# Kernel tuning notes

Measured on AMD Instinct MI355X. Metric: run time of the kernel, lower is better.

Reference implementation:

```python
import jax, jax.numpy as jnp
import numpy as np

B, S, DIM = 8, 1024, 192
D2 = 2 * DIM            # inner width 384
CH = 4                  # cell heads (= qk_size)
HD = D2 // CH           # 96 head dim
NB = D2 // 4            # 96 block-diagonal blocks
BLK = D2 // NB          # block size 4
TAU = float(HD) ** 0.5


def setup_inputs() -> dict:
    key = jax.random.key(0)
    ks = jax.random.split(key, 16)
    r = lambda i, shp, s=0.02: jax.random.normal(ks[i], shp, jnp.float32) * s
    return {
        "x": jax.random.normal(ks[0], (B, S, DIM), jnp.float32),
        "ln_g": jnp.ones((DIM,), jnp.float32), "ln_b": jnp.zeros((DIM,), jnp.float32),
        "w1": r(1, (D2, DIM)), "b1": jnp.zeros((D2,), jnp.float32),
        "w2": r(2, (D2, DIM)), "b2": jnp.zeros((D2,), jnp.float32),
        "conv_w": r(3, (D2, 1, 3), 0.1), "conv_b": jnp.zeros((D2,), jnp.float32),
        "qw": r(4, (NB, BLK, BLK), 0.1), "qb": jnp.zeros((D2,), jnp.float32),
        "kw": r(5, (NB, BLK, BLK), 0.1), "kb": jnp.zeros((D2,), jnp.float32),
        "vw": r(6, (NB, BLK, BLK), 0.1), "vb": jnp.zeros((D2,), jnp.float32),
        "wi": r(7, (CH, 3 * D2)), "bi": jax.random.normal(ks[8], (CH,), jnp.float32) * 0.1,
        "wf": r(9, (CH, 3 * D2)), "bf": jnp.linspace(3.0, 6.0, CH).astype(jnp.float32),
        "gn_g": jnp.ones((D2,), jnp.float32), "gn_b": jnp.zeros((D2,), jnp.float32),
        "wo": r(10, (DIM, D2)), "bo": jnp.zeros((DIM,), jnp.float32),
        "skip": jnp.ones((D2,), jnp.float32),
    }


def _layernorm(x, g, b):
    m = x.mean(-1, keepdims=True)
    v = ((x - m) ** 2).mean(-1, keepdims=True)
    return (x - m) / jnp.sqrt(v + 1e-5) * g + b


def _blockdiag(x, w, b):
    # x: [B,S,D2] -> blocks [B,S,NB,BLK]; w: [NB, out_blk, in_blk]
    bs, sq, _ = x.shape
    y = jnp.einsum('bsni,noi->bsno', x.reshape(bs, sq, NB, BLK), w)
    return y.reshape(bs, sq, D2) + b


def _dwconv(x, w, b):
    # depthwise conv over sequence: x [B,S,C] -> [B,C,S] conv -> [B,S,C]
    y = jax.lax.conv_general_dilated(
        x.transpose(0, 2, 1), w, window_strides=(1,), padding=[(1, 1)],
        dimension_numbers=('NCH', 'OIH', 'NCH'), feature_group_count=D2)
    return y.transpose(0, 2, 1) + b


def _cell(q, k, v, wi, bi, wf, bf, gn_g, gn_b):
    bs, sq, _ = q.shape
    gi = jnp.concatenate([q, k, v], axis=-1)                      # [B,S,3*D2]
    it = jnp.einsum('bsc,hc->bhs', gi, wi) + bi[None, :, None]    # [B,H,S]
    ft = jnp.einsum('bsc,hc->bhs', gi, wf) + bf[None, :, None]
    c = jnp.cumsum(jax.nn.log_sigmoid(ft), axis=-1)               # [B,H,S]
    logm = c[..., :, None] - c[..., None, :]                      # cum[i]-cum[j]
    mask = jnp.tril(jnp.ones((sq, sq), dtype=bool))
    f_act = jnp.where(mask, logm, -jnp.inf)
    dt = f_act + it[:, :, None, :]                                # add itilde over cols
    max_d = jnp.max(dt, axis=-1, keepdims=True)
    dmat = jnp.exp(dt - max_d)                                    # [B,H,S,S]
    qh = q.reshape(bs, sq, CH, HD).transpose(0, 2, 1, 3)
    kh = k.reshape(bs, sq, CH, HD).transpose(0, 2, 1, 3)
    vh = v.reshape(bs, sq, CH, HD).transpose(0, 2, 1, 3)
    ct = jnp.einsum('bhid,bhjd->bhij', qh, kh) * dmat / TAU
    maxit = jnp.maximum(jnp.abs(ct.sum(-1, keepdims=True)), jnp.exp(-max_d))
    h = jnp.einsum('bhij,bhjd->bhid', ct, vh) / (maxit + 1e-6)
    h = h.transpose(0, 2, 1, 3).reshape(bs, sq, CH, HD)           # per-token GroupNorm
    mu = h.mean(-1, keepdims=True)
    var = ((h - mu) ** 2).mean(-1, keepdims=True)
    h = (h - mu) / jnp.sqrt(var + 1e-5)
    h = h * gn_g.reshape(CH, HD) + gn_b.reshape(CH, HD)
    return h.reshape(bs, sq, D2)


def reference(x, ln_g, ln_b, w1, b1, w2, b2, conv_w, conv_b, qw, qb, kw, kb,
              vw, vb, wi, bi, wf, bf, gn_g, gn_b, wo, bo, skip):
    inputs = _layernorm(x, ln_g, ln_b)
    a = inputs @ w1.T + b1                   # [B,S,D2]
    bgate = jax.nn.silu(inputs @ w2.T + b2)  # [B,S,D2]
    qk = jax.nn.silu(_dwconv(a, conv_w, conv_b))
    q = _blockdiag(qk, qw, qb)
    k = _blockdiag(qk, kw, kb)
    v = _blockdiag(a, vw, vb)
    out1 = _cell(q, k, v, wi, bi, wf, bf, gn_g, gn_b)
    out1 = (out1 + skip * qk) * bgate
    out = out1 @ wo.T + bo
    return out + x
```

## Files before the change

### kernel.cpp

```cpp
#include <hip/hip_runtime.h>
#include <cstdint>

#define TAU_ 9.797958971132712f

typedef __attribute__((ext_vector_type(4))) float f32x4;
typedef __attribute__((ext_vector_type(8))) short short8;

#define DEV static __device__ __forceinline__

DEV unsigned short f2bf(float f){
  union { float f; unsigned u; } v; v.f = f;
  unsigned r = v.u + 0x7FFFu + ((v.u >> 16) & 1u);
  return (unsigned short)(r >> 16);
}
DEV float bf2f(unsigned short u){
  union { unsigned u; float f; } v; v.u = ((unsigned)u) << 16; return v.f;
}
DEV unsigned pack2bf(float a, float b){
  unsigned r;
  asm("v_cvt_pk_bf16_f32 %0, %1, %2" : "=v"(r) : "v"(a), "v"(b));
  return r;
}
DEV f32x4 ld_bf4(const unsigned short* p){
  uint2 r = *(const uint2*)p;
  f32x4 o;
  o[0] = bf2f((unsigned short)(r.x & 0xffff));
  o[1] = bf2f((unsigned short)(r.x >> 16));
  o[2] = bf2f((unsigned short)(r.y & 0xffff));
  o[3] = bf2f((unsigned short)(r.y >> 16));
  return o;
}
DEV float siluf_(float x){ return x / (1.f + __expf(-x)); }
DEV float logsigf_(float x){ return fminf(x, 0.f) - log1pf(__expf(-fabsf(x))); }

__global__ __launch_bounds__(256) void k1a_ln(
    const float* __restrict__ x, const float* __restrict__ ln_g, const float* __restrict__ ln_b,
    short* __restrict__ xnbf)
{
  const int tid = threadIdx.x;
  const int t = blockIdx.x * 16 + (tid >> 4);
  const int g = tid & 15;
  const float* xr = x + (long)t * 192 + g * 12;
  f32x4 v0 = *(const f32x4*)(xr);
  f32x4 v1 = *(const f32x4*)(xr + 4);
  f32x4 v2 = *(const f32x4*)(xr + 8);
  float s  = v0[0]+v0[1]+v0[2]+v0[3] + v1[0]+v1[1]+v1[2]+v1[3] + v2[0]+v2[1]+v2[2]+v2[3];
  float sq = v0[0]*v0[0]+v0[1]*v0[1]+v0[2]*v0[2]+v0[3]*v0[3]
           + v1[0]*v1[0]+v1[1]*v1[1]+v1[2]*v1[2]+v1[3]*v1[3]
           + v2[0]*v2[0]+v2[1]*v2[1]+v2[2]*v2[2]+v2[3]*v2[3];
  s  += __shfl_xor(s, 1);  s  += __shfl_xor(s, 2);  s  += __shfl_xor(s, 4);  s  += __shfl_xor(s, 8);
  sq += __shfl_xor(sq, 1); sq += __shfl_xor(sq, 2); sq += __shfl_xor(sq, 4); sq += __shfl_xor(sq, 8);
  const float mean = s * (1.f/192.f);
  const float rstd = rsqrtf(sq * (1.f/192.f) - mean * mean + 1e-5f);
  const int c0 = g * 12;
  f32x4 g0 = *(const f32x4*)(ln_g + c0),     b0 = *(const f32x4*)(ln_b + c0);
  f32x4 g1 = *(const f32x4*)(ln_g + c0 + 4), b1 = *(const f32x4*)(ln_b + c0 + 4);
  f32x4 g2 = *(const f32x4*)(ln_g + c0 + 8), b2 = *(const f32x4*)(ln_b + c0 + 8);
  unsigned pk[6];
  pk[0] = pack2bf((v0[0]-mean)*rstd*g0[0]+b0[0], (v0[1]-mean)*rstd*g0[1]+b0[1]);
  pk[1] = pack2bf((v0[2]-mean)*rstd*g0[2]+b0[2], (v0[3]-mean)*rstd*g0[3]+b0[3]);
  pk[2] = pack2bf((v1[0]-mean)*rstd*g1[0]+b1[0], (v1[1]-mean)*rstd*g1[1]+b1[1]);
  pk[3] = pack2bf((v1[2]-mean)*rstd*g1[2]+b1[2], (v1[3]-mean)*rstd*g1[3]+b1[3]);
  pk[4] = pack2bf((v2[0]-mean)*rstd*g2[0]+b2[0], (v2[1]-mean)*rstd*g2[1]+b2[1]);
  pk[5] = pack2bf((v2[2]-mean)*rstd*g2[2]+b2[2], (v2[3]-mean)*rstd*g2[3]+b2[3]);
  uint2* xo = (uint2*)(xnbf + (long)t * 192 + g * 12);
  xo[0] = make_uint2(pk[0], pk[1]);
  xo[1] = make_uint2(pk[2], pk[3]);
  xo[2] = make_uint2(pk[4], pk[5]);
}

__global__ __launch_bounds__(256) void k1b_gemm(
    const short* __restrict__ xnbf,
    const float* __restrict__ w1, const float* __restrict__ w2,
    const float* __restrict__ b1, const float* __restrict__ b2,
    unsigned short* __restrict__ abf, unsigned short* __restrict__ bgate)
{
  __shared__ short wt[18432];
  const int tid = threadIdx.x;
  const int ntg = blockIdx.x & 7;
  const int t0 = (blockIdx.x >> 3) * 64;
  {
    const float* src = (ntg < 4 ? w1 : w2) + (long)(ntg & 3) * 96 * 192;
    #pragma unroll
    for(int i = 0; i < 9; i++){
      const int u = i * 256 + tid;
      const int row = u / 24;
      const int dst = (u * 16) ^ ((row & 7) << 4);
      f32x4 f0 = *(const f32x4*)(src + u * 8);
      f32x4 f1 = *(const f32x4*)(src + u * 8 + 4);
      uint4 pk;
      pk.x = pack2bf(f0[0], f0[1]); pk.y = pack2bf(f0[2], f0[3]);
      pk.z = pack2bf(f1[0], f1[1]); pk.w = pack2bf(f1[2], f1[3]);
      *(uint4*)((char*)wt + dst) = pk;
    }
  }
  __syncthreads();
  const int widx = tid >> 6, lane = tid & 63, qg = lane >> 4, l16 = lane & 15;
  const int mrow = widx * 16 + l16;
  f32x4 acc[6];
  #pragma unroll
  for(int nt = 0; nt < 6; nt++) acc[nt] = (f32x4){0.f,0.f,0.f,0.f};
  const short* xrow = xnbf + (long)(t0 + mrow) * 192;
  #pragma unroll
  for(int kc = 0; kc < 6; kc++){
    short8 af = *(const short8*)(xrow + kc * 32 + 8 * qg);
    #pragma unroll
    for(int nt = 0; nt < 6; nt++){
      const int row = nt * 16 + l16;
      int byte = row * 384 + (kc * 32 + 8 * qg) * 2;
      byte ^= (row & 7) << 4;
      short8 bfr = *(const short8*)((const char*)wt + byte);
      acc[nt] = __builtin_amdgcn_mfma_f32_16x16x32_bf16(af, bfr, acc[nt], 0, 0, 0);
    }
  }
  const int half = ntg >> 2;
  const float* bias = half ? b2 : b1;
  const int ncol = (ntg & 3) * 96;
  #pragma unroll
  for(int nt = 0; nt < 6; nt++){
    const int n = ncol + nt * 16 + l16;
    const float bs = bias[n];
    #pragma unroll
    for(int r = 0; r < 4; r++){
      const int trow = t0 + widx * 16 + 4 * qg + r;
      float v = acc[nt][r] + bs;
      if(half) bgate[(long)trow * 384 + n] = f2bf(siluf_(v));
      else     abf[(long)trow * 384 + n] = f2bf(v);
    }
  }
}

__global__ __launch_bounds__(256) void k2bv(
    const unsigned short* __restrict__ abf,
    const float* __restrict__ cw, const float* __restrict__ cb,
    const float* __restrict__ qw, const float* __restrict__ qb,
    const float* __restrict__ kw, const float* __restrict__ kb,
    const float* __restrict__ vw, const float* __restrict__ vb,
    unsigned short* __restrict__ qkbf, short* __restrict__ qbf, short* __restrict__ kbf,
    short* __restrict__ vtbf)
{
  __shared__ float vt[64][97];
  const int tid = threadIdx.x;
  const int bh = blockIdx.x >> 4;
  const int b = bh >> 2, h = bh & 3;
  const int s0 = (blockIdx.x & 15) << 6;
  #pragma unroll
  for(int it = 0; it < 6; it++){
    const int f = it * 256 + tid;
    const int sl = f / 24, c4l = f % 24;
    const int c4 = h * 24 + c4l;
    const int s = s0 + sl;
    const long t = (long)b * 1024 + s;
    const long abase = t * 384 + c4 * 4;
    f32x4 am = ld_bf4(abf + abase);
    f32x4 al = (s > 0)    ? ld_bf4(abf + abase - 384) : (f32x4){0.f,0.f,0.f,0.f};
    f32x4 ar = (s < 1023) ? ld_bf4(abf + abase + 384) : (f32x4){0.f,0.f,0.f,0.f};
    f32x4 cw0 = *(const f32x4*)(cw + c4 * 12);
    f32x4 cw1 = *(const f32x4*)(cw + c4 * 12 + 4);
    f32x4 cw2 = *(const f32x4*)(cw + c4 * 12 + 8);
    f32x4 cb4 = *(const f32x4*)(cb + c4 * 4);
    f32x4 in;
    in[0] = siluf_(cb4[0] + al[0]*cw0[0] + am[0]*cw0[1] + ar[0]*cw0[2]);
    in[1] = siluf_(cb4[1] + al[1]*cw0[3] + am[1]*cw1[0] + ar[1]*cw1[1]);
    in[2] = siluf_(cb4[2] + al[2]*cw1[2] + am[2]*cw1[3] + ar[2]*cw2[0]);
    in[3] = siluf_(cb4[3] + al[3]*cw2[1] + am[3]*cw2[2] + ar[3]*cw2[3]);
    {
      uint2 pk; pk.x = pack2bf(in[0], in[1]); pk.y = pack2bf(in[2], in[3]);
      *(uint2*)(qkbf + abase) = pk;
    }
    const long base = ((long)(b * 4 + h) * 1024 + s) * 96 + c4l * 4;
    {
      const float* w = qw + c4 * 16;
      float v0 = qb[c4*4+0] + w[0]*in[0]  + w[1]*in[1]  + w[2]*in[2]  + w[3]*in[3];
      float v1 = qb[c4*4+1] + w[4]*in[0]  + w[5]*in[1]  + w[6]*in[2]  + w[7]*in[3];
      float v2 = qb[c4*4+2] + w[8]*in[0]  + w[9]*in[1]  + w[10]*in[2] + w[11]*in[3];
      float v3 = qb[c4*4+3] + w[12]*in[0] + w[13]*in[1] + w[14]*in[2] + w[15]*in[3];
      uint2 pk; pk.x = pack2bf(v0, v1); pk.y = pack2bf(v2, v3);
      *(uint2*)(qbf + base) = pk;
    }
    {
      const float* w = kw + c4 * 16;
      float v0 = kb[c4*4+0] + w[0]*in[0]  + w[1]*in[1]  + w[2]*in[2]  + w[3]*in[3];
      float v1 = kb[c4*4+1] + w[4]*in[0]  + w[5]*in[1]  + w[6]*in[2]  + w[7]*in[3];
      float v2 = kb[c4*4+2] + w[8]*in[0]  + w[9]*in[1]  + w[10]*in[2] + w[11]*in[3];
      float v3 = kb[c4*4+3] + w[12]*in[0] + w[13]*in[1] + w[14]*in[2] + w[15]*in[3];
      uint2 pk; pk.x = pack2bf(v0, v1); pk.y = pack2bf(v2, v3);
      *(uint2*)(kbf + base) = pk;
    }
    {
      const float* w = vw + c4 * 16;
      #pragma unroll
      for(int o = 0; o < 4; o++){
        float v = vb[c4*4+o] + w[o*4]*am[0] + w[o*4+1]*am[1] + w[o*4+2]*am[2] + w[o*4+3]*am[3];
        vt[sl][c4l * 4 + o] = v;
      }
    }
  }
  __syncthreads();
  #pragma unroll
  for(int it = 0; it < 24; it++){
    const int f = it * 256 + tid;
    const int d = f >> 6, sl = f & 63;
    vtbf[((long)bh * 96 + d) * 1024 + s0 + sl] = (short)f2bf(vt[sl][d]);
  }
}

__global__ __launch_bounds__(256) void k2c_gates(
    const short* __restrict__ qbf, const short* __restrict__ kbf,
    const unsigned short* __restrict__ abf,
    const float* __restrict__ vw, const float* __restrict__ vb,
    const float* __restrict__ wi, const float* __restrict__ bi,
    const float* __restrict__ wf, const float* __restrict__ bff,
    float* __restrict__ itv, float* __restrict__ ftv)
{
  const int tid = threadIdx.x;
  const int lane = tid & 63, widx = tid >> 6;
  const int t = blockIdx.x * 4 + widx;
  const int b = t >> 10, s = t & 1023;
  float pit[4] = {0,0,0,0}, pft[4] = {0,0,0,0};
  for(int j = 0; j < 18; j++){
    const int e = lane + 64 * j;
    float val;
    if(e < 768){
      const int c = (e >= 384) ? e - 384 : e;
      const short* src = (e >= 384) ? kbf : qbf;
      const int h = c / 96, d = c - h * 96;
      val = bf2f((unsigned short)src[((long)(b * 4 + h) * 1024 + s) * 96 + d]);
    } else {
      const int c = e - 768;
      const int c4 = c >> 2, o = c & 3;
      f32x4 in = ld_bf4(abf + (long)t * 384 + c4 * 4);
      const float* w = vw + c4 * 16 + o * 4;
      val = vb[c] + w[0]*in[0] + w[1]*in[1] + w[2]*in[2] + w[3]*in[3];
    }
    #pragma unroll
    for(int h = 0; h < 4; h++){
      pit[h] += val * wi[h * 1152 + e];
      pft[h] += val * wf[h * 1152 + e];
    }
  }
  #pragma unroll
  for(int h = 0; h < 4; h++){
    float vi = pit[h], vf = pft[h];
    #pragma unroll
    for(int m = 1; m < 64; m <<= 1){ vi += __shfl_xor(vi, m); vf += __shfl_xor(vf, m); }
    if(lane == 0){
      itv[((long)(b * 4 + h)) * 1024 + s] = vi + bi[h];
      ftv[((long)(b * 4 + h)) * 1024 + s] = vf + bff[h];
    }
  }
}

__global__ __launch_bounds__(256) void k3_scan(
    const float* __restrict__ itv, const float* __restrict__ ftv,
    float* __restrict__ Ev, float* __restrict__ Rpv, float* __restrict__ dsv)
{
  __shared__ float sb[256];
  const int bh = blockIdx.x, tid = threadIdx.x;
  const long base = (long)bh * 1024 + tid * 4;
  f32x4 f4 = *(const f32x4*)(ftv + base);
  const float l0 = logsigf_(f4[0]);
  const float l1 = logsigf_(f4[1]);
  const float l2 = logsigf_(f4[2]);
  const float l3 = logsigf_(f4[3]);
  float c0 = l0, c1 = l0 + l1, c2 = c1 + l2, c3 = c2 + l3;
  sb[tid] = c3;
  __syncthreads();
  for(int off = 1; off < 256; off <<= 1){
    float mine = sb[tid];
    float oth = (tid >= off) ? sb[tid - off] : 0.f;
    __syncthreads();
    sb[tid] = mine + oth;
    __syncthreads();
  }
  const float excl = (tid > 0) ? sb[tid - 1] : 0.f;
  c0 += excl; c1 += excl; c2 += excl; c3 += excl;
  f32x4 i4 = *(const f32x4*)(itv + base);
  const float m0 = i4[0] - c0, m1 = i4[1] - c1, m2 = i4[2] - c2, m3 = i4[3] - c3;
  const float x1 = fmaxf(m0, m1), x2 = fmaxf(x1, m2), x3 = fmaxf(x2, m3);
  __syncthreads();
  sb[tid] = x3;
  __syncthreads();
  for(int off = 1; off < 256; off <<= 1){
    float mine = sb[tid];
    float oth = (tid >= off) ? sb[tid - off] : -3.4e38f;
    __syncthreads();
    sb[tid] = fmaxf(mine, oth);
    __syncthreads();
  }
  const float exm = (tid > 0) ? sb[tid - 1] : -3.4e38f;
  const float M0 = fmaxf(m0, exm);
  const float M1 = fmaxf(x1, exm);
  const float M2 = fmaxf(x2, exm);
  const float M3 = fmaxf(x3, exm);
  f32x4 e, rp, ds;
  e[0] = __expf(m0); e[1] = __expf(m1); e[2] = __expf(m2); e[3] = __expf(m3);
  rp[0] = __expf(-M0) * (1.f/TAU_); rp[1] = __expf(-M1) * (1.f/TAU_);
  rp[2] = __expf(-M2) * (1.f/TAU_); rp[3] = __expf(-M3) * (1.f/TAU_);
  ds[0] = __expf(-(c0 + M0)); ds[1] = __expf(-(c1 + M1));
  ds[2] = __expf(-(c2 + M2)); ds[3] = __expf(-(c3 + M3));
  *(f32x4*)(Ev  + base) = e;
  *(f32x4*)(Rpv + base) = rp;
  *(f32x4*)(dsv + base) = ds;
}

__global__ __launch_bounds__(256, 2) void k4_attn(
    const short* __restrict__ qbf, const short* __restrict__ kbf, const short* __restrict__ vtbf,
    const float* __restrict__ Ev, const float* __restrict__ Rpv, const float* __restrict__ dsv,
    const float* __restrict__ gn_g, const float* __restrict__ gn_b,
    const unsigned short* __restrict__ qkbf, const unsigned short* __restrict__ bgate,
    const float* __restrict__ skip, short* __restrict__ o1bf)
{
  __shared__ short kbuf[2][64 * 104];
  __shared__ short vbuf[2][96 * 72];
  __shared__ float ebuf[2][64];
  __shared__ short P[4][16][72];
  const int tid = threadIdx.x;
  const int w = tid >> 6, lane = tid & 63, qg = lane >> 4, l16 = lane & 15;
  const int xcd = blockIdx.x & 7, q = blockIdx.x >> 3;
  const int bh = ((q & 3) << 3) | xcd;
  const int qh = q >> 2;
  const int ib = (q < 32) ? (15 - qh) : (qh - 8);
  const int i0w = ib * 64 + w * 16;
  const long qkbase = (long)bh * 1024;
  const int nj = ib + 1;

  short8 qf[3];
  #pragma unroll
  for(int kc = 0; kc < 3; kc++)
    qf[kc] = *(const short8*)(qbf + (qkbase + i0w + l16) * 96 + kc * 32 + 8 * qg);
  const float rp = Rpv[qkbase + i0w + l16];
  const float ds = dsv[qkbase + i0w + l16];

  f32x4 acc[6];
  #pragma unroll
  for(int dt = 0; dt < 6; dt++) acc[dt] = (f32x4){0.f,0.f,0.f,0.f};
  float bp = 0.f;

  const int rK0 = tid / 12,        cK0 = tid % 12;
  const int rK1 = (tid+256) / 12,  cK1 = (tid+256) % 12;
  const int rK2 = (tid+512) / 12,  cK2 = (tid+512) % 12;
  const int dV0 = tid >> 3,        cV0 = tid & 7;
  const int dV1 = (tid+256) >> 3,  cV1 = (tid+256) & 7;
  const int dV2 = (tid+512) >> 3,  cV2 = (tid+512) & 7;
  const bool he = (tid < 16);
  short8 sk0, sk1, sk2, sv0, sv1, sv2; f32x4 se;
  const short* kgb = kbf + qkbase * 96;
  const short* vgb = vtbf + (long)bh * 96 * 1024;

#define STAGE_LOAD(J0)                                              \
  {                                                                 \
    const int j0_ = (J0);                                           \
    sk0 = *(const short8*)(kgb + (j0_ + rK0) * 96 + cK0 * 8);       \
    sk1 = *(const short8*)(kgb + (j0_ + rK1) * 96 + cK1 * 8);       \
    sk2 = *(const short8*)(kgb + (j0_ + rK2) * 96 + cK2 * 8);       \
    sv0 = *(const short8*)(vgb + (long)dV0 * 1024 + j0_ + cV0 * 8); \
    sv1 = *(const short8*)(vgb + (long)dV1 * 1024 + j0_ + cV1 * 8); \
    sv2 = *(const short8*)(vgb + (long)dV2 * 1024 + j0_ + cV2 * 8); \
    if(he) se = *(const f32x4*)(Ev + qkbase + j0_ + tid * 4);       \
  }

#define STAGE_WRITE(B)                                   \
  {                                                      \
    *(short8*)(&kbuf[B][rK0 * 104 + cK0 * 8]) = sk0;     \
    *(short8*)(&kbuf[B][rK1 * 104 + cK1 * 8]) = sk1;     \
    *(short8*)(&kbuf[B][rK2 * 104 + cK2 * 8]) = sk2;     \
    *(short8*)(&vbuf[B][dV0 * 72 + cV0 * 8]) = sv0;      \
    *(short8*)(&vbuf[B][dV1 * 72 + cV1 * 8]) = sv1;      \
    *(short8*)(&vbuf[B][dV2 * 72 + cV2 * 8]) = sv2;      \
    if(he) *(f32x4*)(&ebuf[B][tid * 4]) = se;            \
  }

  STAGE_LOAD(0);
  int cur = 0;
  for(int jt = 0; jt < nj; jt++){
    STAGE_WRITE(cur);
    __syncthreads();
    if(jt + 1 < nj) STAGE_LOAD((jt + 1) * 64);

    const int j0 = jt * 64;
    const bool diag = (jt == nj - 1);
    const int i = i0w + l16;
    __builtin_amdgcn_s_setprio(1);
    #pragma unroll
    for(int jsub = 0; jsub < 4; jsub++){
      f32x4 C = (f32x4){0.f,0.f,0.f,0.f};
      #pragma unroll
      for(int kc = 0; kc < 3; kc++){
        short8 kf = *(const short8*)(&kbuf[cur][(jsub*16 + l16) * 104 + kc * 32 + 8 * qg]);
        C = __builtin_amdgcn_mfma_f32_16x16x32_bf16(kf, qf[kc], C, 0, 0, 0);
      }
      f32x4 e4 = *(const f32x4*)(&ebuf[cur][jsub * 16 + 4 * qg]);
      float v0 = C[0] * e4[0];
      float v1 = C[1] * e4[1];
      float v2 = C[2] * e4[2];
      float v3 = C[3] * e4[3];
      if(diag){
        const int jb = j0 + jsub * 16 + 4 * qg;
        if(jb + 0 > i) v0 = 0.f;
        if(jb + 1 > i) v1 = 0.f;
        if(jb + 2 > i) v2 = 0.f;
        if(jb + 3 > i) v3 = 0.f;
      }
      bp += v0 + v1 + v2 + v3;
      uint2 pw; pw.x = pack2bf(v0, v1); pw.y = pack2bf(v2, v3);
      *(uint2*)(&P[w][l16][jsub * 16 + 4 * qg]) = pw;
    }
    asm volatile("s_waitcnt lgkmcnt(0)" ::: "memory");
    #pragma unroll
    for(int ksub = 0; ksub < 2; ksub++){
      short8 pa = *(const short8*)(&P[w][l16][ksub * 32 + 8 * qg]);
      #pragma unroll
      for(int dt = 0; dt < 6; dt++){
        short8 vf = *(const short8*)(&vbuf[cur][(dt * 16 + l16) * 72 + ksub * 32 + 8 * qg]);
        acc[dt] = __builtin_amdgcn_mfma_f32_16x16x32_bf16(pa, vf, acc[dt], 0, 0, 0);
      }
    }
    __builtin_amdgcn_s_setprio(0);
    cur ^= 1;
  }
#undef STAGE_LOAD
#undef STAGE_WRITE

  const int head = bh & 3, bb = bh >> 2;
  float bsum = bp;
  bsum += __shfl_xor(bsum, 16);
  bsum += __shfl_xor(bsum, 32);
  const float bfull = bsum * rp;
  const float den = fmaxf(fabsf(bfull), ds) + 1e-6f;
  const float sc = rp / den;
  float srow[4];
  #pragma unroll
  for(int r = 0; r < 4; r++) srow[r] = __shfl(sc, 4 * qg + r);
  float hv[6][4], mu[4], rs[4];
  #pragma unroll
  for(int r = 0; r < 4; r++){
    float sm = 0.f, sq = 0.f;
    #pragma unroll
    for(int dt = 0; dt < 6; dt++){
      const float h = acc[dt][r] * srow[r];
      hv[dt][r] = h; sm += h; sq += h * h;
    }
    sm += __shfl_xor(sm, 1); sm += __shfl_xor(sm, 2); sm += __shfl_xor(sm, 4); sm += __shfl_xor(sm, 8);
    sq += __shfl_xor(sq, 1); sq += __shfl_xor(sq, 2); sq += __shfl_xor(sq, 4); sq += __shfl_xor(sq, 8);
    const float m_ = sm * (1.f/96.f);
    mu[r] = m_;
    rs[r] = rsqrtf(sq * (1.f/96.f) - m_ * m_ + 1e-5f);
  }
  __syncthreads();
  short* hstage = &kbuf[0][0];
  #pragma unroll
  for(int dt = 0; dt < 6; dt++){
    const int col = head * 96 + dt * 16 + l16;
    const float g  = gn_g[col];
    const float be = gn_b[col];
    #pragma unroll
    for(int r = 0; r < 4; r++){
      const float hn = (hv[dt][r] - mu[r]) * rs[r] * g + be;
      hstage[(w * 16 + 4 * qg + r) * 104 + dt * 16 + l16] = (short)f2bf(hn);
    }
  }
  __syncthreads();
  #pragma unroll
  for(int u2 = 0; u2 < 3; u2++){
    const int f = u2 * 256 + tid;
    const int row = f / 12, c8 = f % 12;
    const long off = ((long)(bb * 1024 + ib * 64 + row)) * 384 + head * 96 + c8 * 8;
    short8 h8 = *(const short8*)(hstage + row * 104 + c8 * 8);
    short8 q8 = *(const short8*)((const short*)qkbf + off);
    short8 g8 = *(const short8*)((const short*)bgate + off);
    f32x4 s0 = *(const f32x4*)(skip + head * 96 + c8 * 8);
    f32x4 s1 = *(const f32x4*)(skip + head * 96 + c8 * 8 + 4);
    float o[8];
    #pragma unroll
    for(int i = 0; i < 8; i++){
      const float sk = (i < 4) ? s0[i] : s1[i - 4];
      o[i] = (bf2f((unsigned short)h8[i]) + sk * bf2f((unsigned short)q8[i]))
             * bf2f((unsigned short)g8[i]);
    }
    union { short8 s; unsigned u4[4]; } ov;
    ov.u4[0] = pack2bf(o[0], o[1]); ov.u4[1] = pack2bf(o[2], o[3]);
    ov.u4[2] = pack2bf(o[4], o[5]); ov.u4[3] = pack2bf(o[6], o[7]);
    *(short8*)(o1bf + off) = ov.s;
  }
}

__global__ __launch_bounds__(256) void k5_gemm(
    const short* __restrict__ o1bf, const float* __restrict__ wo,
    const float* __restrict__ bo, const float* __restrict__ x, float* __restrict__ out)
{
  __shared__ short wt[18432];
  const int tid = threadIdx.x;
  const int ng = blockIdx.x & 3;
  const int t0 = (blockIdx.x >> 2) * 64;
  {
    const float* src = wo + (long)ng * 48 * 384;
    #pragma unroll
    for(int i = 0; i < 9; i++){
      const int u = i * 256 + tid;
      const int row = u / 48;
      const int dst = (u * 16) ^ ((row & 7) << 4);
      f32x4 f0 = *(const f32x4*)(src + u * 8);
      f32x4 f1 = *(const f32x4*)(src + u * 8 + 4);
      uint4 pk;
      pk.x = pack2bf(f0[0], f0[1]); pk.y = pack2bf(f0[2], f0[3]);
      pk.z = pack2bf(f1[0], f1[1]); pk.w = pack2bf(f1[2], f1[3]);
      *(uint4*)((char*)wt + dst) = pk;
    }
  }
  __syncthreads();
  const int widx = tid >> 6, lane = tid & 63, qg = lane >> 4, l16 = lane & 15;
  f32x4 acc[3];
  #pragma unroll
  for(int nt = 0; nt < 3; nt++) acc[nt] = (f32x4){0.f,0.f,0.f,0.f};
  const short* arow = o1bf + (long)(t0 + widx * 16 + l16) * 384;
  #pragma unroll
  for(int kc = 0; kc < 12; kc++){
    short8 af = *(const short8*)(arow + kc * 32 + 8 * qg);
    #pragma unroll
    for(int nt = 0; nt < 3; nt++){
      const int row = nt * 16 + l16;
      int byte = row * 768 + kc * 64 + qg * 16;
      byte ^= (row & 7) << 4;
      short8 bfr = *(const short8*)((const char*)wt + byte);
      acc[nt] = __builtin_amdgcn_mfma_f32_16x16x32_bf16(af, bfr, acc[nt], 0, 0, 0);
    }
  }
  #pragma unroll
  for(int nt = 0; nt < 3; nt++){
    const int n = ng * 48 + nt * 16 + l16;
    const float b_ = bo[n];
    #pragma unroll
    for(int r = 0; r < 4; r++){
      const int trow = t0 + widx * 16 + 4 * qg + r;
      out[(long)trow * 192 + n] = acc[nt][r] + b_ + x[(long)trow * 192 + n];
    }
  }
}

extern "C" void kernel_launch(void* const* d_in, const int* in_sizes, int n_in,
                              void* d_out, int out_size, void* d_ws, size_t ws_size,
                              hipStream_t stream)
{
  (void)in_sizes; (void)n_in; (void)out_size; (void)ws_size;
  const float* x    = (const float*)d_in[0];
  const float* ln_g = (const float*)d_in[1];
  const float* ln_b = (const float*)d_in[2];
  const float* w1   = (const float*)d_in[3];
  const float* b1   = (const float*)d_in[4];
  const float* w2   = (const float*)d_in[5];
  const float* b2   = (const float*)d_in[6];
  const float* cw   = (const float*)d_in[7];
  const float* cb   = (const float*)d_in[8];
  const float* qw   = (const float*)d_in[9];
  const float* qb   = (const float*)d_in[10];
  const float* kw   = (const float*)d_in[11];
  const float* kb   = (const float*)d_in[12];
  const float* vw   = (const float*)d_in[13];
  const float* vb   = (const float*)d_in[14];
  const float* wi   = (const float*)d_in[15];
  const float* bi   = (const float*)d_in[16];
  const float* wf   = (const float*)d_in[17];
  const float* bff  = (const float*)d_in[18];
  const float* gn_g = (const float*)d_in[19];
  const float* gn_b = (const float*)d_in[20];
  const float* wo   = (const float*)d_in[21];
  const float* bo   = (const float*)d_in[22];
  const float* skip = (const float*)d_in[23];
  float* out = (float*)d_out;

  char* ws = (char*)d_ws;
  unsigned short* abf   = (unsigned short*)(ws + 0);
  unsigned short* bgate = (unsigned short*)(ws + 12582912);
  unsigned short* qkbf  = (unsigned short*)(ws + 25165824);
  short* xnbf  = (short*)(ws + 37748736);
  short* o1bf  = (short*)(ws + 41943040);
  short* qbf   = (short*)(ws + 50331648);
  short* kbf   = (short*)(ws + 56623104);
  short* vtbf  = (short*)(ws + 62914560);
  float* itv   = (float*)(ws + 69648384);
  float* ftv   = (float*)(ws + 69779456);
  float* Ev    = (float*)(ws + 69910528);
  float* Rpv   = (float*)(ws + 70041600);
  float* dsv   = (float*)(ws + 70172672);

  k1a_ln<<<512, 256, 0, stream>>>(x, ln_g, ln_b, xnbf);
  k1b_gemm<<<1024, 256, 0, stream>>>(xnbf, w1, w2, b1, b2, abf, bgate);
  k2bv<<<512, 256, 0, stream>>>(abf, cw, cb, qw, qb, kw, kb, vw, vb, qkbf, qbf, kbf, vtbf);
  k2c_gates<<<2048, 256, 0, stream>>>(qbf, kbf, abf, vw, vb, wi, bi, wf, bff, itv, ftv);
  k3_scan<<<32, 256, 0, stream>>>(itv, ftv, Ev, Rpv, dsv);
  k4_attn<<<512, 256, 0, stream>>>(qbf, kbf, vtbf, Ev, Rpv, dsv, gn_g, gn_b,
                                   qkbf, bgate, skip, o1bf);
  k5_gemm<<<512, 256, 0, stream>>>(o1bf, wo, bo, x, out);
}
```

Measured before the change: 89.10 us.

## Single-buffer K/V LDS tiles in attention kernel and raise occupancy to four blocks

Drops the double-buffered K, V and E shared-memory tiles in the attention kernel in favour of a single buffer. A second barrier at the end of each tile iteration keeps the next write from overwriting data still being read. This roughly halves the LDS footprint, and launch bounds are raised to four blocks per CU so more waves can hide latency. The cost is an extra __syncthreads per tile and a tighter register budget, which may cause spills. Global prefetch into registers still overlaps with compute.

```diff
diff --git a/kernel.cpp b/kernel.cpp
--- a/kernel.cpp
+++ b/kernel.cpp
@@ -304,16 +304,16 @@
   *(f32x4*)(dsv + base) = ds;
 }
 
-__global__ __launch_bounds__(256, 2) void k4_attn(
+__global__ __launch_bounds__(256, 4) void k4_attn(
     const short* __restrict__ qbf, const short* __restrict__ kbf, const short* __restrict__ vtbf,
     const float* __restrict__ Ev, const float* __restrict__ Rpv, const float* __restrict__ dsv,
     const float* __restrict__ gn_g, const float* __restrict__ gn_b,
     const unsigned short* __restrict__ qkbf, const unsigned short* __restrict__ bgate,
     const float* __restrict__ skip, short* __restrict__ o1bf)
 {
-  __shared__ short kbuf[2][64 * 104];
-  __shared__ short vbuf[2][96 * 72];
-  __shared__ float ebuf[2][64];
+  __shared__ short kbuf[64 * 104];
+  __shared__ short vbuf[96 * 72];
+  __shared__ float ebuf[64];
   __shared__ short P[4][16][72];
   const int tid = threadIdx.x;
   const int w = tid >> 6, lane = tid & 63, qg = lane >> 4, l16 = lane & 15;
@@ -360,21 +360,20 @@
     if(he) se = *(const f32x4*)(Ev + qkbase + j0_ + tid * 4);       \
   }
 
-#define STAGE_WRITE(B)                                   \
+#define STAGE_WRITE()                                    \
   {                                                      \
-    *(short8*)(&kbuf[B][rK0 * 104 + cK0 * 8]) = sk0;     \
-    *(short8*)(&kbuf[B][rK1 * 104 + cK1 * 8]) = sk1;     \
-    *(short8*)(&kbuf[B][rK2 * 104 + cK2 * 8]) = sk2;     \
-    *(short8*)(&vbuf[B][dV0 * 72 + cV0 * 8]) = sv0;      \
-    *(short8*)(&vbuf[B][dV1 * 72 + cV1 * 8]) = sv1;      \
-    *(short8*)(&vbuf[B][dV2 * 72 + cV2 * 8]) = sv2;      \
-    if(he) *(f32x4*)(&ebuf[B][tid * 4]) = se;            \
+    *(short8*)(&kbuf[rK0 * 104 + cK0 * 8]) = sk0;        \
+    *(short8*)(&kbuf[rK1 * 104 + cK1 * 8]) = sk1;        \
+    *(short8*)(&kbuf[rK2 * 104 + cK2 * 8]) = sk2;        \
+    *(short8*)(&vbuf[dV0 * 72 + cV0 * 8]) = sv0;         \
+    *(short8*)(&vbuf[dV1 * 72 + cV1 * 8]) = sv1;         \
+    *(short8*)(&vbuf[dV2 * 72 + cV2 * 8]) = sv2;         \
+    if(he) *(f32x4*)(&ebuf[tid * 4]) = se;               \
   }
 
   STAGE_LOAD(0);
-  int cur = 0;
   for(int jt = 0; jt < nj; jt++){
-    STAGE_WRITE(cur);
+    STAGE_WRITE();
     __syncthreads();
     if(jt + 1 < nj) STAGE_LOAD((jt + 1) * 64);
 
@@ -387,10 +386,10 @@
       f32x4 C = (f32x4){0.f,0.f,0.f,0.f};
       #pragma unroll
       for(int kc = 0; kc < 3; kc++){
-        short8 kf = *(const short8*)(&kbuf[cur][(jsub*16 + l16) * 104 + kc * 32 + 8 * qg]);
+        short8 kf = *(const short8*)(&kbuf[(jsub*16 + l16) * 104 + kc * 32 + 8 * qg]);
         C = __builtin_amdgcn_mfma_f32_16x16x32_bf16(kf, qf[kc], C, 0, 0, 0);
       }
-      f32x4 e4 = *(const f32x4*)(&ebuf[cur][jsub * 16 + 4 * qg]);
+      f32x4 e4 = *(const f32x4*)(&ebuf[jsub * 16 + 4 * qg]);
       float v0 = C[0] * e4[0];
       float v1 = C[1] * e4[1];
       float v2 = C[2] * e4[2];
@@ -412,12 +411,12 @@
       short8 pa = *(const short8*)(&P[w][l16][ksub * 32 + 8 * qg]);
       #pragma unroll
       for(int dt = 0; dt < 6; dt++){
-        short8 vf = *(const short8*)(&vbuf[cur][(dt * 16 + l16) * 72 + ksub * 32 + 8 * qg]);
+        short8 vf = *(const short8*)(&vbuf[(dt * 16 + l16) * 72 + ksub * 32 + 8 * qg]);
         acc[dt] = __builtin_amdgcn_mfma_f32_16x16x32_bf16(pa, vf, acc[dt], 0, 0, 0);
       }
     }
     __builtin_amdgcn_s_setprio(0);
-    cur ^= 1;
+    __syncthreads();
   }
 #undef STAGE_LOAD
 #undef STAGE_WRITE
@@ -447,8 +446,7 @@
     mu[r] = m_;
     rs[r] = rsqrtf(sq * (1.f/96.f) - m_ * m_ + 1e-5f);
   }
-  __syncthreads();
-  short* hstage = &kbuf[0][0];
+  short* hstage = &kbuf[0];
   #pragma unroll
   for(int dt = 0; dt < 6; dt++){
     const int col = head * 96 + dt * 16 + l16;
```

After: 93.51 us. +5.0%, slower.

## Compute gate projections with bf16 MFMA and a materialized V buffer

Applied to the files above, without the earlier changes.

The gate kernel, which had one wave per token doing scalar dot products and shuffle reductions, is rewritten to use 16x16x32 bf16 MFMA. Each block loads the wi/wf gate weights into LDS as bf16 and covers 64 tokens. To feed it, k2bv now also writes the block-diagonal V projection to a token-major bf16 buffer, so the gate kernel no longer recomputes V from `a`. In exchange, k2bv writes one extra buffer, the grid shrinks to 128 blocks, and the V values and gate weights are rounded to bf16 inside the gate computation.

```diff
diff --git a/kernel.cpp b/kernel.cpp
--- a/kernel.cpp
+++ b/kernel.cpp
@@ -137,7 +137,7 @@
     const float* __restrict__ kw, const float* __restrict__ kb,
     const float* __restrict__ vw, const float* __restrict__ vb,
     unsigned short* __restrict__ qkbf, short* __restrict__ qbf, short* __restrict__ kbf,
-    short* __restrict__ vtbf)
+    short* __restrict__ vbf, short* __restrict__ vtbf)
 {
   __shared__ float vt[64][97];
   const int tid = threadIdx.x;
@@ -189,11 +189,15 @@
     }
     {
       const float* w = vw + c4 * 16;
+      float vv[4];
       #pragma unroll
       for(int o = 0; o < 4; o++){
         float v = vb[c4*4+o] + w[o*4]*am[0] + w[o*4+1]*am[1] + w[o*4+2]*am[2] + w[o*4+3]*am[3];
+        vv[o] = v;
         vt[sl][c4l * 4 + o] = v;
       }
+      uint2 pk; pk.x = pack2bf(vv[0], vv[1]); pk.y = pack2bf(vv[2], vv[3]);
+      *(uint2*)(vbf + abase) = pk;
     }
   }
   __syncthreads();
@@ -206,47 +210,48 @@
 }
 
 __global__ __launch_bounds__(256) void k2c_gates(
-    const short* __restrict__ qbf, const short* __restrict__ kbf,
-    const unsigned short* __restrict__ abf,
-    const float* __restrict__ vw, const float* __restrict__ vb,
+    const short* __restrict__ qbf, const short* __restrict__ kbf, const short* __restrict__ vbf,
     const float* __restrict__ wi, const float* __restrict__ bi,
     const float* __restrict__ wf, const float* __restrict__ bff,
     float* __restrict__ itv, float* __restrict__ ftv)
 {
+  __shared__ short wg[8 * 1160];
   const int tid = threadIdx.x;
-  const int lane = tid & 63, widx = tid >> 6;
-  const int t = blockIdx.x * 4 + widx;
-  const int b = t >> 10, s = t & 1023;
-  float pit[4] = {0,0,0,0}, pft[4] = {0,0,0,0};
-  for(int j = 0; j < 18; j++){
-    const int e = lane + 64 * j;
-    float val;
-    if(e < 768){
-      const int c = (e >= 384) ? e - 384 : e;
-      const short* src = (e >= 384) ? kbf : qbf;
-      const int h = c / 96, d = c - h * 96;
-      val = bf2f((unsigned short)src[((long)(b * 4 + h) * 1024 + s) * 96 + d]);
-    } else {
-      const int c = e - 768;
-      const int c4 = c >> 2, o = c & 3;
-      f32x4 in = ld_bf4(abf + (long)t * 384 + c4 * 4);
-      const float* w = vw + c4 * 16 + o * 4;
-      val = vb[c] + w[0]*in[0] + w[1]*in[1] + w[2]*in[2] + w[3]*in[3];
-    }
-    #pragma unroll
-    for(int h = 0; h < 4; h++){
-      pit[h] += val * wi[h * 1152 + e];
-      pft[h] += val * wf[h * 1152 + e];
-    }
-  }
-  #pragma unroll
-  for(int h = 0; h < 4; h++){
-    float vi = pit[h], vf = pft[h];
-    #pragma unroll
-    for(int m = 1; m < 64; m <<= 1){ vi += __shfl_xor(vi, m); vf += __shfl_xor(vf, m); }
-    if(lane == 0){
-      itv[((long)(b * 4 + h)) * 1024 + s] = vi + bi[h];
-      ftv[((long)(b * 4 + h)) * 1024 + s] = vf + bff[h];
+  const int t0 = blockIdx.x * 64;
+  #pragma unroll
+  for(int i = 0; i < 9; i++){
+    const int u = i * 256 + tid;
+    const int row = u / 288, col4 = u % 288;
+    const float* src = ((row < 4) ? wi + row * 1152 : wf + (row - 4) * 1152) + col4 * 4;
+    f32x4 v = *(const f32x4*)src;
+    uint2 pk; pk.x = pack2bf(v[0], v[1]); pk.y = pack2bf(v[2], v[3]);
+    *(uint2*)(&wg[row * 1160 + col4 * 4]) = pk;
+  }
+  __syncthreads();
+  const int w = tid >> 6, lane = tid & 63, qg = lane >> 4, l16 = lane & 15;
+  const int tw = t0 + w * 16;
+  const int tA = tw + l16;
+  const int b = tA >> 10, s = tA & 1023;
+  f32x4 acc = (f32x4){0.f,0.f,0.f,0.f};
+  #pragma unroll
+  for(int kc = 0; kc < 36; kc++){
+    const int blk = kc / 3;
+    const int off = (kc % 3) * 32 + qg * 8;
+    short8 af;
+    if(blk < 4)      af = *(const short8*)(qbf + ((long)(b*4+blk)*1024 + s)*96 + off);
+    else if(blk < 8) af = *(const short8*)(kbf + ((long)(b*4+blk-4)*1024 + s)*96 + off);
+    else             af = *(const short8*)(vbf + (long)tA*384 + (blk-8)*96 + off);
+    short8 bf8 = *(const short8*)(&wg[(l16 & 7) * 1160 + kc * 32 + qg * 8]);
+    acc = __builtin_amdgcn_mfma_f32_16x16x32_bf16(af, bf8, acc, 0, 0, 0);
+  }
+  if(l16 < 8){
+    const int gh = l16 & 3;
+    const float bias = (l16 < 4) ? bi[gh] : bff[gh];
+    float* dst = (l16 < 4) ? itv : ftv;
+    #pragma unroll
+    for(int r = 0; r < 4; r++){
+      const int t = tw + 4 * qg + r;
+      dst[((long)((t >> 10) * 4 + gh)) * 1024 + (t & 1023)] = acc[r] + bias;
     }
   }
 }
@@ -571,6 +576,7 @@
 
   char* ws = (char*)d_ws;
   unsigned short* abf   = (unsigned short*)(ws + 0);
+  short* vbf   = (short*)(ws + 6291456);
   unsigned short* bgate = (unsigned short*)(ws + 12582912);
   unsigned short* qkbf  = (unsigned short*)(ws + 25165824);
   short* xnbf  = (short*)(ws + 37748736);
@@ -586,8 +592,8 @@
 
   k1a_ln<<<512, 256, 0, stream>>>(x, ln_g, ln_b, xnbf);
   k1b_gemm<<<1024, 256, 0, stream>>>(xnbf, w1, w2, b1, b2, abf, bgate);
-  k2bv<<<512, 256, 0, stream>>>(abf, cw, cb, qw, qb, kw, kb, vw, vb, qkbf, qbf, kbf, vtbf);
-  k2c_gates<<<2048, 256, 0, stream>>>(qbf, kbf, abf, vw, vb, wi, bi, wf, bff, itv, ftv);
+  k2bv<<<512, 256, 0, stream>>>(abf, cw, cb, qw, qb, kw, kb, vw, vb, qkbf, qbf, kbf, vbf, vtbf);
+  k2c_gates<<<128, 256, 0, stream>>>(qbf, kbf, vbf, wi, bi, wf, bff, itv, ftv);
   k3_scan<<<32, 256, 0, stream>>>(itv, ftv, Ev, Rpv, dsv);
   k4_attn<<<512, 256, 0, stream>>>(qbf, kbf, vtbf, Ev, Rpv, dsv, gn_g, gn_b,
                                    qkbf, bgate, skip, o1bf);
```

New measurement: 78.85 us. -11.5%, faster.
